# Performance work log

Measured on AMD Instinct MI355X. Metric: run time of the kernel, lower is better.

Reference implementation:

```python
import jax, jax.numpy as jnp
import numpy as np

ROPE_THETA = 10000.0

def rope(x):
    # RoPE over the FULL model_dim (applied pre head-split, as in the source),
    # interleaved even/odd pairs. x: [B, S, D]
    B, S, D = x.shape
    half = D // 2
    inv_freq = 1.0 / (ROPE_THETA ** (jnp.arange(half, dtype=jnp.float32) * 2.0 / D))
    ang = jnp.arange(S, dtype=jnp.float32)[:, None] * inv_freq[None, :]  # [S, half]
    cos, sin = jnp.cos(ang), jnp.sin(ang)
    x1, x2 = x[..., 0::2], x[..., 1::2]
    r1 = x1 * cos - x2 * sin
    r2 = x1 * sin + x2 * cos
    return jnp.stack([r1, r2], axis=-1).reshape(B, S, D)


def setup_inputs() -> dict:
    key = jax.random.key(0)
    ks = jax.random.split(key, 9)
    B, S, D = 4, 2048, 768
    w = 0.02
    return {
        "X":  jax.random.normal(ks[0], (B, S, D), dtype=jnp.float32),
        "Wq": jax.random.normal(ks[1], (D, D), dtype=jnp.float32) * w,
        "bq": jnp.zeros((D,), dtype=jnp.float32),
        "Wk": jax.random.normal(ks[2], (D, D), dtype=jnp.float32) * w,
        "bk": jnp.zeros((D,), dtype=jnp.float32),
        "Wv": jax.random.normal(ks[3], (D, D), dtype=jnp.float32) * w,
        "bv": jnp.zeros((D,), dtype=jnp.float32),
        "Wo": jax.random.normal(ks[4], (D, D), dtype=jnp.float32) * w,
        "bo": jnp.zeros((D,), dtype=jnp.float32),
    }


def reference(X, Wq, bq, Wk, bk, Wv, bv, Wo, bo):
    NUM_HEADS = 12
    B, S, D = X.shape
    hd = D // NUM_HEADS

    q = rope(X @ Wq + bq)   # RoPE applied pre-split on full model_dim
    k = rope(X @ Wk + bk)
    v = X @ Wv + bv

    # Contiguous per-head slices == reshape to [B, S, H, hd]
    qh = q.reshape(B, S, NUM_HEADS, hd)
    kh = k.reshape(B, S, NUM_HEADS, hd)
    vh = v.reshape(B, S, NUM_HEADS, hd)

    scores = jnp.einsum('bqhd,bkhd->bhqk', qh, kh) / jnp.sqrt(jnp.float32(hd))
    causal = jnp.tril(jnp.ones((S, S), dtype=bool))
    scores = jnp.where(causal[None, None, :, :], scores, -jnp.inf)
    weights = jax.nn.softmax(scores, axis=-1)
    out = jnp.einsum('bhqk,bkhd->bqhd', weights, vh).reshape(B, S, D)
    return out @ Wo + bo
```

## Files before the change

kernel.cpp:

```cpp
#include <hip/hip_runtime.h>
#include <math.h>

#define D_MODEL 768
#define NUM_HEADS 12
#define HEAD_DIM 64
#define SEQ 2048
#define BATCH 4
#define MROWS (BATCH * SEQ)
#define HALF_D (D_MODEL / 2)

typedef __bf16    bf16x8 __attribute__((ext_vector_type(8)));
typedef _Float16  f16x4  __attribute__((ext_vector_type(4)));
typedef float     f32x4  __attribute__((ext_vector_type(4)));

__device__ __forceinline__ void gload_lds16(const void* gp, void* lp) {
    __builtin_amdgcn_global_load_lds(
        (const __attribute__((address_space(1))) unsigned int*)gp,
        (__attribute__((address_space(3))) unsigned int*)lp, 16, 0, 0);
}

__global__ __launch_bounds__(256)
void prep(const float* __restrict__ X, __bf16* __restrict__ Xb,
          const float* __restrict__ W0, const float* __restrict__ W1,
          const float* __restrict__ W2, const float* __restrict__ W3,
          __bf16* __restrict__ T0, __bf16* __restrict__ T1,
          __bf16* __restrict__ T2, __bf16* __restrict__ T3)
{
    __shared__ float t[64][65];
    const int n   = blockIdx.x;
    const int tid = threadIdx.x;

    if (n < 3072) {
        size_t i = ((size_t)n * 256 + tid) * 8;
        float4 u = *(const float4*)(X + i);
        float4 v = *(const float4*)(X + i + 4);
        bf16x8 o;
        o[0]=(__bf16)u.x; o[1]=(__bf16)u.y; o[2]=(__bf16)u.z; o[3]=(__bf16)u.w;
        o[4]=(__bf16)v.x; o[5]=(__bf16)v.y; o[6]=(__bf16)v.z; o[7]=(__bf16)v.w;
        *(bf16x8*)(Xb + i) = o;
    } else {
        int m = n - 3072;
        int z = m / 144;
        int rem = m - z * 144;
        int by = rem / 12, bx = rem % 12;
        const float* W = z == 0 ? W0 : z == 1 ? W1 : z == 2 ? W2 : W3;
        __bf16*      T = z == 0 ? T0 : z == 1 ? T1 : z == 2 ? T2 : T3;

        const int r0 = by * 64, c0 = bx * 64;
        const int lx = tid & 63, g = tid >> 6;

        #pragma unroll
        for (int rr = 0; rr < 16; ++rr) {
            int r = g * 16 + rr;
            t[r][lx] = W[(size_t)(r0 + r) * D_MODEL + c0 + lx];
        }
        __syncthreads();

        const int nn = tid >> 2;
        const int kb = (tid & 3) * 16;
        bf16x8 o1, o2;
        #pragma unroll
        for (int mm = 0; mm < 8; ++mm) o1[mm] = (__bf16)t[kb + mm][nn];
        #pragma unroll
        for (int mm = 0; mm < 8; ++mm) o2[mm] = (__bf16)t[kb + 8 + mm][nn];
        __bf16* dst = T + (size_t)(c0 + nn) * D_MODEL + r0 + kb;
        *(bf16x8*)dst       = o1;
        *(bf16x8*)(dst + 8) = o2;
    }
}

__global__ __launch_bounds__(256)
void qkv_gemm(const __bf16* __restrict__ Xb,
              const __bf16* __restrict__ Wqt, const __bf16* __restrict__ Wkt,
              const __bf16* __restrict__ Wvt,
              const float* __restrict__ bq, const float* __restrict__ bk,
              const float* __restrict__ bv,
              __bf16* __restrict__ Qb, __bf16* __restrict__ Kb,
              _Float16* __restrict__ Vtb)
{
    __shared__ bf16x8 Asf[3][8][64];
    __shared__ bf16x8 Bsf[3][8][64];

    const int tid  = threadIdx.x;
    const int wv   = tid >> 6;
    const int ln   = tid & 63;
    const int t15  = ln & 15;
    const int quad = ln >> 4;
    const int wr = wv >> 1, wc = wv & 1;

    const int lin = blockIdx.x;
    const int c   = lin >> 6;
    const int r   = lin & 63;
    const int which = c / 6;
    const int col0  = (c % 6) * 128;
    const int row0  = r * 128;

    const __bf16* Wt  = which == 0 ? Wqt : which == 1 ? Wkt : Wvt;
    const float* bias = which == 0 ? bq  : which == 1 ? bk  : bv;

    f32x4 acc[4][4];
    #pragma unroll
    for (int i = 0; i < 4; ++i)
        #pragma unroll
        for (int j = 0; j < 4; ++j) acc[i][j] = (f32x4){0.f,0.f,0.f,0.f};

    const __bf16* a0 = Xb + (size_t)(row0 + 16 * wv       + t15) * D_MODEL + 8 * quad;
    const __bf16* a1 = Xb + (size_t)(row0 + 16 * (wv + 4) + t15) * D_MODEL + 8 * quad;
    const __bf16* b0 = Wt + (size_t)(col0 + 16 * wv       + t15) * D_MODEL + 8 * quad;
    const __bf16* b1 = Wt + (size_t)(col0 + 16 * (wv + 4) + t15) * D_MODEL + 8 * quad;

    auto stage = [&](int buf, int k0) {
        gload_lds16(a0 + k0, &Asf[buf][wv][0]);
        gload_lds16(a1 + k0, &Asf[buf][wv + 4][0]);
        gload_lds16(b0 + k0, &Bsf[buf][wv][0]);
        gload_lds16(b1 + k0, &Bsf[buf][wv + 4][0]);
    };

    stage(0, 0);
    stage(1, 32);
    stage(2, 64);

    const int NT = D_MODEL / 32;
    int cur = 0;
    for (int t = 0; t < NT; ++t) {
        if (t + 2 < NT)      { asm volatile("s_waitcnt vmcnt(8)" ::: "memory"); }
        else if (t + 1 < NT) { asm volatile("s_waitcnt vmcnt(4)" ::: "memory"); }
        else                 { asm volatile("s_waitcnt vmcnt(0)" ::: "memory"); }
        __builtin_amdgcn_s_barrier();

        bf16x8 af[4], bfr[4];
        #pragma unroll
        for (int i = 0; i < 4; ++i) af[i]  = Asf[cur][4 * wr + i][ln];
        #pragma unroll
        for (int j = 0; j < 4; ++j) bfr[j] = Bsf[cur][4 * wc + j][ln];
        #pragma unroll
        for (int i = 0; i < 4; ++i)
            #pragma unroll
            for (int j = 0; j < 4; ++j)
                acc[i][j] = __builtin_amdgcn_mfma_f32_16x16x32_bf16(af[i], bfr[j], acc[i][j], 0, 0, 0);

        asm volatile("s_waitcnt lgkmcnt(0)" ::: "memory");
        __builtin_amdgcn_s_barrier();
        if (t + 3 < NT) stage(cur, 32 * (t + 3));
        cur = (cur == 2) ? 0 : cur + 1;
    }

    if (which < 2) {
        const float oscale = (which == 0) ? 0.125f : 1.0f;
        __bf16* dst = which ? Kb : Qb;
        #pragma unroll
        for (int i = 0; i < 4; ++i) {
            const int rowb = row0 + 64 * wr + 16 * i + 4 * quad;
            const int s0   = rowb & (SEQ - 1);
            #pragma unroll
            for (int j = 0; j < 4; ++j) {
                const int col = col0 + 64 * wc + 16 * j + t15;
                const float bval = bias[col];
                const int ne = col & ~1;
                const float fr = __expf((float)ne * (-9.210340371976184f / 768.0f));
                const float cf = __cosf(fr), sf = __sinf(fr);
                const float sgn = (col & 1) ? 1.0f : -1.0f;
                float ang = (float)s0 * fr;
                float ca = __cosf(ang), sa = __sinf(ang);
                #pragma unroll
                for (int rr = 0; rr < 4; ++rr) {
                    const int rw = rowb + rr;
                    float val  = acc[i][j][rr] + bval;
                    float part = __shfl_xor(val, 1, 64);
                    dst[(size_t)rw * D_MODEL + col] = (__bf16)((val * ca + part * sgn * sa) * oscale);
                    float cn = ca * cf - sa * sf;
                    sa = sa * cf + ca * sf;
                    ca = cn;
                }
            }
        }
    } else {
        #pragma unroll
        for (int i = 0; i < 4; ++i) {
            const int rowb = row0 + 64 * wr + 16 * i + 4 * quad;
            #pragma unroll
            for (int j = 0; j < 4; ++j) {
                const int col = col0 + 64 * wc + 16 * j + t15;
                const float bval = bias[col];
                const int h = col >> 6, d = col & 63;
                const int bidx = rowb >> 11, s = rowb & (SEQ - 1);
                f16x4 pk;
                #pragma unroll
                for (int rr = 0; rr < 4; ++rr) pk[rr] = (_Float16)(acc[i][j][rr] + bval);
                *(f16x4*)(Vtb + ((size_t)(bidx * NUM_HEADS + h) * 64 + d) * SEQ + s) = pk;
            }
        }
    }
}

__global__ __launch_bounds__(256)
void out_gemm(const __bf16* __restrict__ Ab, const __bf16* __restrict__ Wt,
              const float* __restrict__ bias, float* __restrict__ Cout)
{
    __shared__ bf16x8 Asf[3][4][64];
    __shared__ bf16x8 Bsf[3][8][64];

    const int tid  = threadIdx.x;
    const int wv   = tid >> 6;
    const int ln   = tid & 63;
    const int t15  = ln & 15;
    const int quad = ln >> 4;
    const int wr = wv >> 1, wc = wv & 1;

    const int lin  = blockIdx.x;
    const int col0 = (lin >> 7) * 128;
    const int row0 = (lin & 127) * 64;

    f32x4 acc[2][4];
    #pragma unroll
    for (int i = 0; i < 2; ++i)
        #pragma unroll
        for (int j = 0; j < 4; ++j) acc[i][j] = (f32x4){0.f,0.f,0.f,0.f};

    auto stage = [&](int buf, int k0) {
        #pragma unroll
        for (int u = 0; u < 3; ++u) {
            const int id = wv * 3 + u;
            if (id < 4) {
                const __bf16* src = Ab + (size_t)(row0 + 16 * id + t15) * D_MODEL
                                       + k0 + 8 * quad;
                gload_lds16(src, &Asf[buf][id][0]);
            } else {
                const int w = id - 4;
                const __bf16* src = Wt + (size_t)(col0 + 16 * w + t15) * D_MODEL
                                       + k0 + 8 * quad;
                gload_lds16(src, &Bsf[buf][w][0]);
            }
        }
    };

    stage(0, 0);
    stage(1, 32);
    stage(2, 64);

    const int NT = D_MODEL / 32;
    int cur = 0;
    for (int t = 0; t < NT; ++t) {
        if (t + 2 < NT)      { asm volatile("s_waitcnt vmcnt(6)" ::: "memory"); }
        else if (t + 1 < NT) { asm volatile("s_waitcnt vmcnt(3)" ::: "memory"); }
        else                 { asm volatile("s_waitcnt vmcnt(0)" ::: "memory"); }
        __builtin_amdgcn_s_barrier();

        bf16x8 af[2], bfr[4];
        #pragma unroll
        for (int i = 0; i < 2; ++i) af[i]  = Asf[cur][2 * wr + i][ln];
        #pragma unroll
        for (int j = 0; j < 4; ++j) bfr[j] = Bsf[cur][4 * wc + j][ln];
        #pragma unroll
        for (int i = 0; i < 2; ++i)
            #pragma unroll
            for (int j = 0; j < 4; ++j)
                acc[i][j] = __builtin_amdgcn_mfma_f32_16x16x32_bf16(af[i], bfr[j], acc[i][j], 0, 0, 0);

        asm volatile("s_waitcnt lgkmcnt(0)" ::: "memory");
        __builtin_amdgcn_s_barrier();
        if (t + 3 < NT) stage(cur, 32 * (t + 3));
        cur = (cur == 2) ? 0 : cur + 1;
    }

    #pragma unroll
    for (int i = 0; i < 2; ++i) {
        const int rowb = row0 + 32 * wr + 16 * i + 4 * quad;
        #pragma unroll
        for (int j = 0; j < 4; ++j) {
            const int col = col0 + 64 * wc + 16 * j + t15;
            const float bval = bias[col];
            #pragma unroll
            for (int rr = 0; rr < 4; ++rr)
                Cout[(size_t)(rowb + rr) * D_MODEL + col] = acc[i][j][rr] + bval;
        }
    }
}

__device__ __forceinline__ void attn_tile(
    const bf16x8 (*Kbuf)[64], const _Float16* Vbuf ,
    bf16x8 aq0, bf16x8 aq1,
    f32x4* o, float& lacc,
    int ln, int t15, int quad, int j0, int qglob, bool domask)
{
    f32x4 s[4];
    #pragma unroll
    for (int c = 0; c < 4; ++c) {
        s[c] = (f32x4){0.f, 0.f, 0.f, 0.f};
        s[c] = __builtin_amdgcn_mfma_f32_16x16x32_bf16(Kbuf[c][ln],     aq0, s[c], 0, 0, 0);
        s[c] = __builtin_amdgcn_mfma_f32_16x16x32_bf16(Kbuf[4 + c][ln], aq1, s[c], 0, 0, 0);
    }

    f16x4 pf[4];
    #pragma unroll
    for (int c = 0; c < 4; ++c)
        #pragma unroll
        for (int r = 0; r < 4; ++r) {
            float e = __expf(s[c][r]);
            if (domask && (j0 + 16 * c + 4 * quad + r > qglob)) e = 0.f;
            lacc += e;
            pf[c][r] = (_Float16)e;
        }

    #pragma unroll
    for (int c = 0; c < 4; ++c) {
        const int lv = 16 * (2 * (c & 1) + (quad >> 1)) + t15;
        const int jb = 4 * (quad & 1);
        #pragma unroll
        for (int cd = 0; cd < 4; ++cd) {
            f16x4 vf = *(const f16x4*)&Vbuf[(size_t)(4 * (c >> 1) + cd) * 512 + lv * 8 + jb];
            o[cd] = __builtin_amdgcn_mfma_f32_16x16x16f16(pf[c], vf, o[cd], 0, 0, 0);
        }
    }
}

__global__ __launch_bounds__(512)
void attn_flash(const __bf16* __restrict__ Q, const __bf16* __restrict__ K,
                const _Float16* __restrict__ Vt, __bf16* __restrict__ O)
{
    __shared__ bf16x8   Kf[2][8][64];
    __shared__ _Float16 Vh[2][8][512];

    const int tid  = threadIdx.x;
    const int wv   = tid >> 6;
    const int ln   = tid & 63;
    const int t15  = ln & 15;
    const int quad = ln >> 4;

    const int n  = blockIdx.x;
    const int qt = 15 - (n / 48);
    const int bh = n % 48;
    const int b  = bh / NUM_HEADS;
    const int h  = bh % NUM_HEADS;
    const int q0 = qt * 128;
    const int nt = (q0 >> 6) + 2;

    bf16x8 aq0, aq1;
    {
        const __bf16* qs = Q + (size_t)(b * SEQ + q0 + 16 * wv + t15) * D_MODEL + h * 64 + 8 * quad;
        aq0 = *(const bf16x8*)qs;
        aq1 = *(const bf16x8*)(qs + 32);
    }

    const __bf16*   kp = K  + ((size_t)b * SEQ + 16 * (wv & 3) + t15) * D_MODEL
                            + h * 64 + 32 * (wv >> 2) + 8 * quad;
    const _Float16* vp = Vt + ((size_t)bh * 64 + 16 * (wv & 3) + t15) * SEQ
                            + 32 * (wv >> 2) + 8 * quad;

    f32x4 o[4];
    #pragma unroll
    for (int c = 0; c < 4; ++c) o[c] = (f32x4){0.f,0.f,0.f,0.f};
    float lacc = 0.f;
    const int qglob = q0 + 16 * wv + t15;
    const int wmax  = q0 + 16 * wv + 15;

    gload_lds16(kp, &Kf[0][wv][0]);
    gload_lds16(vp, &Vh[0][wv][0]);

    int cur = 0;
    for (int it = 0; it < nt; ++it) {
        __syncthreads();
        if (it + 1 < nt) {
            const int jn = (it + 1) * 64;
            gload_lds16(kp + (size_t)jn * D_MODEL, &Kf[cur ^ 1][wv][0]);
            gload_lds16(vp + jn,                   &Vh[cur ^ 1][wv][0]);
        }
        const int j0 = it * 64;
        if (j0 <= wmax) {
            const bool domask = (j0 + 63) > (q0 + 16 * wv);
            attn_tile(Kf[cur], &Vh[cur][0][0], aq0, aq1, o, lacc,
                      ln, t15, quad, j0, qglob, domask);
        }
        cur ^= 1;
    }

    lacc += __shfl_xor(lacc, 16, 64);
    lacc += __shfl_xor(lacc, 32, 64);

    float inv[4];
    #pragma unroll
    for (int r = 0; r < 4; ++r)
        inv[r] = 1.0f / __shfl(lacc, 4 * quad + r, 64);

    #pragma unroll
    for (int c = 0; c < 4; ++c)
        #pragma unroll
        for (int r = 0; r < 4; ++r) {
            int row = q0 + 16 * wv + 4 * quad + r;
            O[(size_t)(b * SEQ + row) * D_MODEL + h * 64 + 16 * c + t15] = (__bf16)(o[c][r] * inv[r]);
        }
}

extern "C" void kernel_launch(void* const* d_in, const int* in_sizes, int n_in,
                              void* d_out, int out_size, void* d_ws, size_t ws_size,
                              hipStream_t stream) {
    const float* X  = (const float*)d_in[0];
    const float* Wq = (const float*)d_in[1];
    const float* bq = (const float*)d_in[2];
    const float* Wk = (const float*)d_in[3];
    const float* bk = (const float*)d_in[4];
    const float* Wv = (const float*)d_in[5];
    const float* bv = (const float*)d_in[6];
    const float* Wo = (const float*)d_in[7];
    const float* bo = (const float*)d_in[8];
    float* out = (float*)d_out;

    const size_t BSD = (size_t)MROWS * D_MODEL;
    const size_t WSZ = (size_t)D_MODEL * D_MODEL;

    __bf16*   Xb  = (__bf16*)d_ws;
    __bf16*   Qb  = Xb  + BSD;
    __bf16*   Kb  = Qb  + BSD;
    _Float16* Vtb = (_Float16*)(Kb + BSD);
    __bf16*   Ob  = (__bf16*)(Vtb + BSD);
    __bf16*   Wqt = Ob  + BSD;
    __bf16*   Wkt = Wqt + WSZ;
    __bf16*   Wvt = Wkt + WSZ;
    __bf16*   Wot = Wvt + WSZ;

    prep<<<3648, 256, 0, stream>>>(X, Xb, Wq, Wk, Wv, Wo, Wqt, Wkt, Wvt, Wot);

    qkv_gemm<<<1152, 256, 0, stream>>>(Xb, Wqt, Wkt, Wvt, bq, bk, bv, Qb, Kb, Vtb);

    attn_flash<<<768, 512, 0, stream>>>(Qb, Kb, Vtb, Ob);

    out_gemm<<<768, 256, 0, stream>>>(Ob, Wot, bo, out);
}
```

Baseline: 260.5 us.

## Restructure QKV GEMM to 8 waves with double-buffered 64-wide K steps

```diff
diff --git a/kernel.cpp b/kernel.cpp
--- a/kernel.cpp
+++ b/kernel.cpp
@@ -69,7 +69,7 @@
     }
 }
 
-__global__ __launch_bounds__(256)
+__global__ __launch_bounds__(512, 4)
 void qkv_gemm(const __bf16* __restrict__ Xb,
               const __bf16* __restrict__ Wqt, const __bf16* __restrict__ Wkt,
               const __bf16* __restrict__ Wvt,
@@ -78,15 +78,15 @@
               __bf16* __restrict__ Qb, __bf16* __restrict__ Kb,
               _Float16* __restrict__ Vtb)
 {
-    __shared__ bf16x8 Asf[3][8][64];
-    __shared__ bf16x8 Bsf[3][8][64];
+    __shared__ bf16x8 Asf[2][2][8][64];
+    __shared__ bf16x8 Bsf[2][2][8][64];
 
     const int tid  = threadIdx.x;
     const int wv   = tid >> 6;
     const int ln   = tid & 63;
     const int t15  = ln & 15;
     const int quad = ln >> 4;
-    const int wr = wv >> 1, wc = wv & 1;
+    const int wr = wv >> 2, wc = wv & 3;
 
     const int lin = blockIdx.x;
     const int c   = lin >> 6;
@@ -98,63 +98,73 @@
     const __bf16* Wt  = which == 0 ? Wqt : which == 1 ? Wkt : Wvt;
     const float* bias = which == 0 ? bq  : which == 1 ? bk  : bv;
 
-    f32x4 acc[4][4];
+    f32x4 acc[4][2];
     #pragma unroll
     for (int i = 0; i < 4; ++i)
         #pragma unroll
-        for (int j = 0; j < 4; ++j) acc[i][j] = (f32x4){0.f,0.f,0.f,0.f};
-
-    const __bf16* a0 = Xb + (size_t)(row0 + 16 * wv       + t15) * D_MODEL + 8 * quad;
-    const __bf16* a1 = Xb + (size_t)(row0 + 16 * (wv + 4) + t15) * D_MODEL + 8 * quad;
-    const __bf16* b0 = Wt + (size_t)(col0 + 16 * wv       + t15) * D_MODEL + 8 * quad;
-    const __bf16* b1 = Wt + (size_t)(col0 + 16 * (wv + 4) + t15) * D_MODEL + 8 * quad;
+        for (int j = 0; j < 2; ++j) acc[i][j] = (f32x4){0.f,0.f,0.f,0.f};
+
+    const __bf16* seg[4];
+    bf16x8*       dst[4];
+    #pragma unroll
+    for (int u = 0; u < 4; ++u) {
+        const int id  = wv * 4 + u;
+        const int isB = id >> 4;
+        const int s   = id & 15;
+        const int ks  = s >> 3, slot = s & 7;
+        const __bf16* base = isB
+            ? Wt + (size_t)(col0 + 16 * slot + t15) * D_MODEL
+            : Xb + (size_t)(row0 + 16 * slot + t15) * D_MODEL;
+        seg[u] = base + 32 * ks + 8 * quad;
+        dst[u] = isB ? &Bsf[0][ks][slot][0] : &Asf[0][ks][slot][0];
+    }
 
     auto stage = [&](int buf, int k0) {
-        gload_lds16(a0 + k0, &Asf[buf][wv][0]);
-        gload_lds16(a1 + k0, &Asf[buf][wv + 4][0]);
-        gload_lds16(b0 + k0, &Bsf[buf][wv][0]);
-        gload_lds16(b1 + k0, &Bsf[buf][wv + 4][0]);
+        #pragma unroll
+        for (int u = 0; u < 4; ++u)
+            gload_lds16(seg[u] + k0, dst[u] + buf * 1024);
     };
 
     stage(0, 0);
-    stage(1, 32);
-    stage(2, 64);
-
-    const int NT = D_MODEL / 32;
+    stage(1, 64);
+
+    const int NT = D_MODEL / 64;
     int cur = 0;
     for (int t = 0; t < NT; ++t) {
-        if (t + 2 < NT)      { asm volatile("s_waitcnt vmcnt(8)" ::: "memory"); }
-        else if (t + 1 < NT) { asm volatile("s_waitcnt vmcnt(4)" ::: "memory"); }
-        else                 { asm volatile("s_waitcnt vmcnt(0)" ::: "memory"); }
+        if (t < NT - 1) { asm volatile("s_waitcnt vmcnt(4)" ::: "memory"); }
+        else            { asm volatile("s_waitcnt vmcnt(0)" ::: "memory"); }
         __builtin_amdgcn_s_barrier();
 
-        bf16x8 af[4], bfr[4];
-        #pragma unroll
-        for (int i = 0; i < 4; ++i) af[i]  = Asf[cur][4 * wr + i][ln];
-        #pragma unroll
-        for (int j = 0; j < 4; ++j) bfr[j] = Bsf[cur][4 * wc + j][ln];
-        #pragma unroll
-        for (int i = 0; i < 4; ++i)
-            #pragma unroll
-            for (int j = 0; j < 4; ++j)
-                acc[i][j] = __builtin_amdgcn_mfma_f32_16x16x32_bf16(af[i], bfr[j], acc[i][j], 0, 0, 0);
+        #pragma unroll
+        for (int ks = 0; ks < 2; ++ks) {
+            bf16x8 af[4], bfr[2];
+            #pragma unroll
+            for (int i = 0; i < 4; ++i) af[i]  = Asf[cur][ks][4 * wr + i][ln];
+            #pragma unroll
+            for (int j = 0; j < 2; ++j) bfr[j] = Bsf[cur][ks][2 * wc + j][ln];
+            #pragma unroll
+            for (int i = 0; i < 4; ++i)
+                #pragma unroll
+                for (int j = 0; j < 2; ++j)
+                    acc[i][j] = __builtin_amdgcn_mfma_f32_16x16x32_bf16(af[i], bfr[j], acc[i][j], 0, 0, 0);
+        }
 
         asm volatile("s_waitcnt lgkmcnt(0)" ::: "memory");
         __builtin_amdgcn_s_barrier();
-        if (t + 3 < NT) stage(cur, 32 * (t + 3));
-        cur = (cur == 2) ? 0 : cur + 1;
+        if (t + 2 < NT) stage(cur, 64 * (t + 2));
+        cur ^= 1;
     }
 
     if (which < 2) {
         const float oscale = (which == 0) ? 0.125f : 1.0f;
-        __bf16* dst = which ? Kb : Qb;
+        __bf16* dstq = which ? Kb : Qb;
         #pragma unroll
         for (int i = 0; i < 4; ++i) {
             const int rowb = row0 + 64 * wr + 16 * i + 4 * quad;
             const int s0   = rowb & (SEQ - 1);
             #pragma unroll
-            for (int j = 0; j < 4; ++j) {
-                const int col = col0 + 64 * wc + 16 * j + t15;
+            for (int j = 0; j < 2; ++j) {
+                const int col = col0 + 32 * wc + 16 * j + t15;
                 const float bval = bias[col];
                 const int ne = col & ~1;
                 const float fr = __expf((float)ne * (-9.210340371976184f / 768.0f));
@@ -167,7 +177,7 @@
                     const int rw = rowb + rr;
                     float val  = acc[i][j][rr] + bval;
                     float part = __shfl_xor(val, 1, 64);
-                    dst[(size_t)rw * D_MODEL + col] = (__bf16)((val * ca + part * sgn * sa) * oscale);
+                    dstq[(size_t)rw * D_MODEL + col] = (__bf16)((val * ca + part * sgn * sa) * oscale);
                     float cn = ca * cf - sa * sf;
                     sa = sa * cf + ca * sf;
                     ca = cn;
@@ -179,8 +189,8 @@
         for (int i = 0; i < 4; ++i) {
             const int rowb = row0 + 64 * wr + 16 * i + 4 * quad;
             #pragma unroll
-            for (int j = 0; j < 4; ++j) {
-                const int col = col0 + 64 * wc + 16 * j + t15;
+            for (int j = 0; j < 2; ++j) {
+                const int col = col0 + 32 * wc + 16 * j + t15;
                 const float bval = bias[col];
                 const int h = col >> 6, d = col & 63;
                 const int bidx = rowb >> 11, s = rowb & (SEQ - 1);
@@ -420,7 +430,7 @@
 
     prep<<<3648, 256, 0, stream>>>(X, Xb, Wq, Wk, Wv, Wo, Wqt, Wkt, Wvt, Wot);
 
-    qkv_gemm<<<1152, 256, 0, stream>>>(Xb, Wqt, Wkt, Wvt, bq, bk, bv, Qb, Kb, Vtb);
+    qkv_gemm<<<1152, 512, 0, stream>>>(Xb, Wqt, Wkt, Wvt, bq, bk, bv, Qb, Kb, Vtb);
 
     attn_flash<<<768, 512, 0, stream>>>(Qb, Kb, Vtb, Ob);
 
```

Result: faster. 238.4 us (-8.5%).
